# Kernel tuning notes

Measured on AMD Instinct MI355X. Metric: run time of the kernel, lower is better.

The kernel has to match this reference:

```python
import jax, jax.numpy as jnp
import numpy as np

B, S, D, H = 2, 2048, 1024, 16
DK = D // H


def setup_inputs() -> dict:
    key = jax.random.key(0)
    ks = jax.random.split(key, 12)
    lim = 1.0 / np.sqrt(D)
    def lin(kw, kb):
        W = jax.random.uniform(kw, (D, D), jnp.float32, -lim, lim)
        b = jax.random.uniform(kb, (D,), jnp.float32, -lim, lim)
        return W, b
    Wq, bq = lin(ks[0], ks[1])
    Wk, bk = lin(ks[2], ks[3])
    Wv, bv = lin(ks[4], ks[5])
    Wo, bo = lin(ks[6], ks[7])
    Q = jax.random.normal(ks[8], (B, S, D), jnp.float32)
    K = jax.random.normal(ks[9], (B, S, D), jnp.float32)
    V = jax.random.normal(ks[10], (B, S, D), jnp.float32)
    # causal mask, broadcastable to (B, H, S, S)
    mask = jnp.broadcast_to(jnp.tril(jnp.ones((S, S), jnp.bool_))[None, None], (B, 1, S, S))
    return {"Q": Q, "K": K, "V": V, "mask": mask,
            "Wq": Wq, "bq": bq, "Wk": Wk, "bk": bk,
            "Wv": Wv, "bv": bv, "Wo": Wo, "bo": bo}


def reference(Q, K, V, mask, Wq, bq, Wk, bk, Wv, bv, Wo, bo):
    def split(x):  # (B,S,D) -> (B,H,S,DK)
        return x.reshape(B, S, H, DK).transpose(0, 2, 1, 3)
    q = split(Q @ Wq.T + bq)
    k = split(K @ Wk.T + bk)
    v = split(V @ Wv.T + bv)
    scores = jnp.einsum('bhqd,bhkd->bhqk', q, k) / jnp.sqrt(jnp.float32(DK))
    scores = jnp.where(mask, scores, jnp.float32(-1e9))
    probs = jax.nn.softmax(scores, axis=-1)
    out = jnp.einsum('bhqk,bhkd->bhqd', probs, v)  # (B,H,S,DK)
    out = out.transpose(0, 2, 1, 3).reshape(B, S, D)
    return out @ Wo.T + bo
```

## Files before the change

kernel.cpp:

```cpp
#include <hip/hip_runtime.h>

#define S_LEN 2048
#define D_DIM 1024
#define H_NUM 16
#define DK_DIM 64
#define BATCH 2
#define M_TOT (BATCH * S_LEN)
#define XSZ 4194304
#define WSZ 1048576
#define SCALE_LOG2 0.18033688f

typedef __bf16 bf16x8 __attribute__((ext_vector_type(8)));
typedef float f32x4 __attribute__((ext_vector_type(4)));
typedef unsigned short u16;
typedef unsigned short u16x8 __attribute__((ext_vector_type(8)));

__device__ inline u16 f2bf(float f) {
  union { float f; unsigned u; } v; v.f = f;
  unsigned u = v.u;
  return (u16)((u + 0x7FFFu + ((u >> 16) & 1u)) >> 16);
}

typedef const __attribute__((address_space(1))) unsigned int gu32;
typedef __attribute__((address_space(3))) unsigned int lu32;
__device__ inline void glds16(const u16* g, u16* l) {
  __builtin_amdgcn_global_load_lds((gu32*)g, (lu32*)l, 16, 0, 0);
}

__global__ __launch_bounds__(256)
void convert_kernel(const float* __restrict__ Q, const float* __restrict__ K,
                    const float* __restrict__ V, const float* __restrict__ Wq,
                    const float* __restrict__ Wk, const float* __restrict__ Wv,
                    const float* __restrict__ Wo, u16* __restrict__ Xb,
                    u16* __restrict__ Wb) {
  const size_t e = ((size_t)blockIdx.x * 256 + threadIdx.x) * 8;
  const float* src;
  u16* dst;
  size_t off;
  if (e < 3ull * XSZ) {
    const int a = (int)(e >> 22);
    src = (a == 0) ? Q : (a == 1) ? K : V;
    off = e - ((size_t)a << 22);
    dst = Xb + e;
  } else {
    const size_t ew = e - 3ull * XSZ;
    const int a = (int)(ew >> 20);
    src = (a == 0) ? Wq : (a == 1) ? Wk : (a == 2) ? Wv : Wo;
    off = ew - ((size_t)a << 20);
    dst = Wb + ew;
  }
  const float4 v0 = *reinterpret_cast<const float4*>(&src[off]);
  const float4 v1 = *reinterpret_cast<const float4*>(&src[off + 4]);
  u16x8 w;
  w[0] = f2bf(v0.x); w[1] = f2bf(v0.y); w[2] = f2bf(v0.z); w[3] = f2bf(v0.w);
  w[4] = f2bf(v1.x); w[5] = f2bf(v1.y); w[6] = f2bf(v1.z); w[7] = f2bf(v1.w);
  *reinterpret_cast<u16x8*>(dst) = w;
}

__global__ __launch_bounds__(256)
void proj_kernel(const u16* __restrict__ Qb, const u16* __restrict__ Kb,
                 const u16* __restrict__ Vb, const u16* __restrict__ Wqb,
                 const u16* __restrict__ Wkb, const u16* __restrict__ Wvb,
                 const float* __restrict__ bq, const float* __restrict__ bk,
                 const float* __restrict__ bv, u16* __restrict__ qh,
                 u16* __restrict__ kh, u16* __restrict__ vt) {
  const int f = blockIdx.x + 32 * blockIdx.y + 256 * blockIdx.z;
  const int swz = (f & 7) * 96 + (f >> 3);
  const int z = swz >> 8;
  const int bx = swz & 31, by = (swz >> 5) & 7;

  const u16* A  = (z == 0) ? Qb : (z == 1) ? Kb : Vb;
  const u16* Bw = (z == 0) ? Wqb : (z == 1) ? Wkb : Wvb;
  const float* bias = (z == 0) ? bq : (z == 1) ? bk : bv;
  u16* out = (z == 0) ? qh : (z == 1) ? kh : vt;
  const float oscale = (z == 0) ? SCALE_LOG2 : 1.0f;

  __shared__ __align__(16) u16 Asm[128 * 64];
  __shared__ __align__(16) u16 Bsm[128 * 64];

  const int tid = threadIdx.x;
  const int m0 = bx * 128, n0 = by * 128;
  const int wid = tid >> 6, lane = tid & 63;
  const int col = lane & 15, quad = lane >> 4;
  const int wm = (wid >> 1) * 64, wn = (wid & 1) * 64;

  const int lr = lane >> 3;
  const int lc = (lane & 7) ^ lr;
  const u16* gA = A + (size_t)(m0 + 32 * wid + lr) * D_DIM + lc * 8;
  const u16* gB = Bw + (size_t)(n0 + 32 * wid + lr) * D_DIM + lc * 8;

  f32x4 acc[4][4];
  const f32x4 zero4 = {0.f, 0.f, 0.f, 0.f};
  for (int i = 0; i < 4; i++)
    for (int j = 0; j < 4; j++) acc[i][j] = zero4;

  for (int k0 = 0; k0 < D_DIM; k0 += 64) {
    __syncthreads();
    for (int j = 0; j < 4; j++) {
      glds16(gA + (size_t)j * 8 * D_DIM + k0, &Asm[(32 * wid + 8 * j) * 64]);
      glds16(gB + (size_t)j * 8 * D_DIM + k0, &Bsm[(32 * wid + 8 * j) * 64]);
    }
    __syncthreads();

    bf16x8 af[4][2], bfm[4][2];
    for (int i = 0; i < 4; i++) {
      const int row = wm + i * 16 + col;
      const int r7 = row & 7;
      af[i][0] = *reinterpret_cast<const bf16x8*>(&Asm[row * 64 + ((quad ^ r7) * 8)]);
      af[i][1] = *reinterpret_cast<const bf16x8*>(&Asm[row * 64 + (((quad + 4) ^ r7) * 8)]);
    }
    for (int j = 0; j < 4; j++) {
      const int row = wn + j * 16 + col;
      const int r7 = row & 7;
      bfm[j][0] = *reinterpret_cast<const bf16x8*>(&Bsm[row * 64 + ((quad ^ r7) * 8)]);
      bfm[j][1] = *reinterpret_cast<const bf16x8*>(&Bsm[row * 64 + (((quad + 4) ^ r7) * 8)]);
    }
    if (z == 2) {
      for (int h = 0; h < 2; h++)
        for (int i = 0; i < 4; i++)
          for (int j = 0; j < 4; j++)
            acc[i][j] = __builtin_amdgcn_mfma_f32_16x16x32_bf16(
                af[i][h], bfm[j][h], acc[i][j], 0, 0, 0);
    } else {
      for (int h = 0; h < 2; h++)
        for (int i = 0; i < 4; i++)
          for (int j = 0; j < 4; j++)
            acc[i][j] = __builtin_amdgcn_mfma_f32_16x16x32_bf16(
                bfm[j][h], af[i][h], acc[i][j], 0, 0, 0);
    }
  }

  if (z != 2) {
    float4 b4[4];
    for (int j = 0; j < 4; j++)
      b4[j] = *reinterpret_cast<const float4*>(&bias[n0 + wn + j * 16 + quad * 4]);
    for (int i = 0; i < 4; i++) {
      const int token = m0 + wm + i * 16 + col;
      const int b = token >> 11, s = token & (S_LEN - 1);
      for (int j = 0; j < 4; j++) {
        const int gnb = n0 + wn + j * 16 + quad * 4;
        const int h = gnb >> 6, dk = gnb & 63;
        ushort4 w;
        w.x = f2bf((acc[i][j][0] + b4[j].x) * oscale);
        w.y = f2bf((acc[i][j][1] + b4[j].y) * oscale);
        w.z = f2bf((acc[i][j][2] + b4[j].z) * oscale);
        w.w = f2bf((acc[i][j][3] + b4[j].w) * oscale);
        *reinterpret_cast<ushort4*>(
            &out[((size_t)(b * H_NUM + h) * S_LEN + s) * DK_DIM + dk]) = w;
      }
    }
  } else {
    float bb[4];
    for (int j = 0; j < 4; j++) bb[j] = bias[n0 + wn + j * 16 + col];
    for (int i = 0; i < 4; i++) {
      const int token0 = m0 + wm + i * 16 + quad * 4;
      const int b = token0 >> 11, s0 = token0 & (S_LEN - 1);
      for (int j = 0; j < 4; j++) {
        const int gn = n0 + wn + j * 16 + col;
        const int h = gn >> 6, dk = gn & 63;
        ushort4 w;
        w.x = f2bf(acc[i][j][0] + bb[j]);
        w.y = f2bf(acc[i][j][1] + bb[j]);
        w.z = f2bf(acc[i][j][2] + bb[j]);
        w.w = f2bf(acc[i][j][3] + bb[j]);
        *reinterpret_cast<ushort4*>(
            &out[((size_t)(b * H_NUM + h) * DK_DIM + dk) * S_LEN + s0]) = w;
      }
    }
  }
}

__global__ __launch_bounds__(256)
void attn_kernel(const u16* __restrict__ qh, const u16* __restrict__ kh,
                 const u16* __restrict__ vt, u16* __restrict__ ctx) {
  __shared__ __align__(16) u16 Ksm[2][64 * 64];
  __shared__ __align__(16) u16 Vsm[2][64 * 64];
  __shared__ __align__(16) u16 Psm[4][16][72];

  const int tid  = threadIdx.x;
  const int flat = blockIdx.x;
  const int qb   = 31 - (flat >> 5);
  const int bh   = flat & 31;
  const int wid  = tid >> 6;
  const int lane = tid & 63;
  const int col  = lane & 15;
  const int quad = lane >> 4;
  const int r7   = col & 7;

  const int lr = lane >> 3;
  const int lc = (lane & 7) ^ lr;
  const u16* kbase = kh + ((size_t)bh * S_LEN + 16 * wid + lr) * DK_DIM + lc * 8;
  const u16* vbase = vt + ((size_t)bh * DK_DIM + 16 * wid + lr) * S_LEN + lc * 8;

  const f32x4 zero4 = {0.f, 0.f, 0.f, 0.f};
  const int b_ = bh >> 4, h_ = bh & 15;

  const int nt = qb + 1;
  const int qrow_w = qb * 64 + wid * 16;
  const int qg = qrow_w + col;

  bf16x8 qB[2];
  {
    const u16* qp = &qh[((size_t)bh * S_LEN + qg) * DK_DIM + quad * 8];
    qB[0] = *reinterpret_cast<const bf16x8*>(qp);
    qB[1] = *reinterpret_cast<const bf16x8*>(qp + 32);
  }

  glds16(kbase, &Ksm[0][(16 * wid) * 64]);
  glds16(kbase + 8 * DK_DIM, &Ksm[0][(16 * wid + 8) * 64]);
  glds16(vbase, &Vsm[0][(16 * wid) * 64]);
  glds16(vbase + (size_t)8 * S_LEN, &Vsm[0][(16 * wid + 8) * 64]);

  float l_ = 0.f;
  f32x4 o[4];
  for (int dm = 0; dm < 4; dm++) o[dm] = zero4;

  for (int tt = 0; tt < nt; tt++) {
    const int b = tt & 1;
    __syncthreads();

    if (tt + 1 < nt) {
      const int nkv = (tt + 1) * 64;
      u16* kd = &Ksm[b ^ 1][(16 * wid) * 64];
      u16* vd = &Vsm[b ^ 1][(16 * wid) * 64];
      glds16(kbase + (size_t)nkv * DK_DIM, kd);
      glds16(kbase + (size_t)(nkv + 8) * DK_DIM, kd + 8 * 64);
      glds16(vbase + nkv, vd);
      glds16(vbase + (size_t)8 * S_LEN + nkv, vd + 8 * 64);
    }

    const int kv0 = tt * 64;
    f32x4 s[4];
    __builtin_amdgcn_s_setprio(1);
    for (int nc = 0; nc < 4; nc++) {
      const int row = nc * 16 + col;
      const bf16x8 kA0 = *reinterpret_cast<const bf16x8*>(
          &Ksm[b][row * 64 + ((quad ^ r7) * 8)]);
      const bf16x8 kA1 = *reinterpret_cast<const bf16x8*>(
          &Ksm[b][row * 64 + (((quad + 4) ^ r7) * 8)]);
      f32x4 acc = zero4;
      acc = __builtin_amdgcn_mfma_f32_16x16x32_bf16(kA0, qB[0], acc, 0, 0, 0);
      acc = __builtin_amdgcn_mfma_f32_16x16x32_bf16(kA1, qB[1], acc, 0, 0, 0);
      s[nc] = acc;
    }
    __builtin_amdgcn_s_setprio(0);

    const bool domask = (kv0 + 63 > qrow_w);
    for (int nc = 0; nc < 4; nc++) {
      const int kvb = kv0 + nc * 16 + quad * 4;
      float p[4];
      for (int r = 0; r < 4; r++) {
        float e = __builtin_amdgcn_exp2f(s[nc][r]);
        if (domask && (kvb + r > qg)) e = 0.f;
        p[r] = e;
      }
      unsigned u0 = __float_as_uint(p[0]), u1 = __float_as_uint(p[1]);
      unsigned u2 = __float_as_uint(p[2]), u3 = __float_as_uint(p[3]);
      l_ += __uint_as_float(u0 & 0xffff0000u);
      l_ += __uint_as_float(u1 & 0xffff0000u);
      l_ += __uint_as_float(u2 & 0xffff0000u);
      l_ += __uint_as_float(u3 & 0xffff0000u);
      uint2 pw;
      pw.x = __builtin_amdgcn_perm(u1, u0, 0x07060302);
      pw.y = __builtin_amdgcn_perm(u3, u2, 0x07060302);
      *reinterpret_cast<uint2*>(&Psm[wid][col][nc * 16 + quad * 4]) = pw;
    }

    asm volatile("s_waitcnt lgkmcnt(0)" ::: "memory");

    bf16x8 pB[2];
    pB[0] = *reinterpret_cast<const bf16x8*>(&Psm[wid][col][quad * 8]);
    pB[1] = *reinterpret_cast<const bf16x8*>(&Psm[wid][col][32 + quad * 8]);
    __builtin_amdgcn_s_setprio(1);
    for (int dm = 0; dm < 4; dm++) {
      const int row = dm * 16 + col;
      const bf16x8 vA0 = *reinterpret_cast<const bf16x8*>(
          &Vsm[b][row * 64 + ((quad ^ r7) * 8)]);
      const bf16x8 vA1 = *reinterpret_cast<const bf16x8*>(
          &Vsm[b][row * 64 + (((quad + 4) ^ r7) * 8)]);
      o[dm] = __builtin_amdgcn_mfma_f32_16x16x32_bf16(vA0, pB[0], o[dm], 0, 0, 0);
      o[dm] = __builtin_amdgcn_mfma_f32_16x16x32_bf16(vA1, pB[1], o[dm], 0, 0, 0);
    }
    __builtin_amdgcn_s_setprio(0);
  }

  float rs = l_;
  rs += __shfl_xor(rs, 16);
  rs += __shfl_xor(rs, 32);
  const float inv = 1.0f / rs;
  for (int dm = 0; dm < 4; dm++) {
    ushort4 w;
    w.x = f2bf(o[dm][0] * inv);
    w.y = f2bf(o[dm][1] * inv);
    w.z = f2bf(o[dm][2] * inv);
    w.w = f2bf(o[dm][3] * inv);
    *reinterpret_cast<ushort4*>(
        &ctx[((size_t)b_ * S_LEN + qg) * D_DIM + h_ * DK_DIM + dm * 16 +
             quad * 4]) = w;
  }
}

__global__ __launch_bounds__(256)
void outproj_kernel(const u16* __restrict__ ctx, const u16* __restrict__ Wob,
                    const float* __restrict__ bo, float* __restrict__ out) {
  __shared__ __align__(16) u16 Asm[2][64 * 64];
  __shared__ __align__(16) u16 Bsm[2][128 * 64];

  const int f = blockIdx.x + 64 * blockIdx.y;
  const int swz = (f & 7) * 64 + (f >> 3);
  const int m0 = (swz & 63) * 64, n0 = (swz >> 6) * 128;

  const int tid = threadIdx.x;
  const int wid = tid >> 6, lane = tid & 63;
  const int col = lane & 15, quad = lane >> 4;

  const int lr = lane >> 3;
  const int lc = (lane & 7) ^ lr;
  const u16* gA = ctx + (size_t)(m0 + 16 * wid + lr) * D_DIM + lc * 8;
  const u16* gB = Wob + (size_t)(n0 + 32 * wid + lr) * D_DIM + lc * 8;

  f32x4 acc[4][2];
  const f32x4 zero4 = {0.f, 0.f, 0.f, 0.f};
  for (int i = 0; i < 4; i++)
    for (int j = 0; j < 2; j++) acc[i][j] = zero4;

  for (int j = 0; j < 2; j++)
    glds16(gA + (size_t)j * 8 * D_DIM, &Asm[0][(16 * wid + 8 * j) * 64]);
  for (int j = 0; j < 4; j++)
    glds16(gB + (size_t)j * 8 * D_DIM, &Bsm[0][(32 * wid + 8 * j) * 64]);

  for (int ks = 0; ks < 16; ks++) {
    const int b = ks & 1;
    __syncthreads();

    if (ks + 1 < 16) {
      const int k1 = (ks + 1) * 64;
      for (int j = 0; j < 2; j++)
        glds16(gA + (size_t)j * 8 * D_DIM + k1,
               &Asm[b ^ 1][(16 * wid + 8 * j) * 64]);
      for (int j = 0; j < 4; j++)
        glds16(gB + (size_t)j * 8 * D_DIM + k1,
               &Bsm[b ^ 1][(32 * wid + 8 * j) * 64]);
    }

    bf16x8 af[4][2], bfm[2][2];
    for (int i = 0; i < 4; i++) {
      const int row = i * 16 + col;
      const int r7 = row & 7;
      af[i][0] = *reinterpret_cast<const bf16x8*>(&Asm[b][row * 64 + ((quad ^ r7) * 8)]);
      af[i][1] = *reinterpret_cast<const bf16x8*>(&Asm[b][row * 64 + (((quad + 4) ^ r7) * 8)]);
    }
    for (int j = 0; j < 2; j++) {
      const int row = 32 * wid + j * 16 + col;
      const int r7 = row & 7;
      bfm[j][0] = *reinterpret_cast<const bf16x8*>(&Bsm[b][row * 64 + ((quad ^ r7) * 8)]);
      bfm[j][1] = *reinterpret_cast<const bf16x8*>(&Bsm[b][row * 64 + (((quad + 4) ^ r7) * 8)]);
    }
    for (int h = 0; h < 2; h++)
      for (int i = 0; i < 4; i++)
        for (int j = 0; j < 2; j++)
          acc[i][j] = __builtin_amdgcn_mfma_f32_16x16x32_bf16(
              bfm[j][h], af[i][h], acc[i][j], 0, 0, 0);
  }

  float4 b4[2];
  for (int j = 0; j < 2; j++)
    b4[j] = *reinterpret_cast<const float4*>(
        &bo[n0 + 32 * wid + j * 16 + quad * 4]);
  for (int i = 0; i < 4; i++) {
    const int token = m0 + i * 16 + col;
    for (int j = 0; j < 2; j++) {
      const int gnb = n0 + 32 * wid + j * 16 + quad * 4;
      float4 v;
      v.x = acc[i][j][0] + b4[j].x;
      v.y = acc[i][j][1] + b4[j].y;
      v.z = acc[i][j][2] + b4[j].z;
      v.w = acc[i][j][3] + b4[j].w;
      *reinterpret_cast<float4*>(&out[(size_t)token * D_DIM + gnb]) = v;
    }
  }
}

extern "C" void kernel_launch(void* const* d_in, const int* in_sizes, int n_in,
                              void* d_out, int out_size, void* d_ws,
                              size_t ws_size, hipStream_t stream) {
  const float* Q  = (const float*)d_in[0];
  const float* K  = (const float*)d_in[1];
  const float* V  = (const float*)d_in[2];
  const float* Wq = (const float*)d_in[4];
  const float* bq = (const float*)d_in[5];
  const float* Wk = (const float*)d_in[6];
  const float* bk = (const float*)d_in[7];
  const float* Wv = (const float*)d_in[8];
  const float* bv = (const float*)d_in[9];
  const float* Wo = (const float*)d_in[10];
  const float* bo = (const float*)d_in[11];
  float* out = (float*)d_out;

  u16* qh  = (u16*)d_ws;
  u16* kh  = qh + XSZ;
  u16* vt  = kh + XSZ;
  u16* Qb  = vt + XSZ;
  u16* ctx = Qb;
  u16* Kb  = Qb + XSZ;
  u16* Vb  = Kb + XSZ;
  u16* Wqb = Vb + XSZ;
  u16* Wkb = Wqb + WSZ;
  u16* Wvb = Wkb + WSZ;
  u16* Wob = Wvb + WSZ;

  convert_kernel<<<(3 * XSZ + 4 * WSZ) / (256 * 8), 256, 0, stream>>>(
      Q, K, V, Wq, Wk, Wv, Wo, Qb, Wqb);

  proj_kernel<<<dim3(M_TOT / 128, D_DIM / 128, 3), 256, 0, stream>>>(
      Qb, Kb, Vb, Wqb, Wkb, Wvb, bq, bk, bv, qh, kh, vt);

  attn_kernel<<<dim3(1024), 256, 0, stream>>>(qh, kh, vt, ctx);

  outproj_kernel<<<dim3(M_TOT / 64, D_DIM / 128), 256, 0, stream>>>(ctx, Wob,
                                                                    bo, out);
}
```

Measured before the change: 260.5 us.

## Drop block swizzles, XOR-swizzle P tile, reorder causal query blocks

Removes the XCD-aware block-index swizzles in the projection and output-projection kernels and goes back to plain grid mapping. The attention kernel's P scratch tile loses its row padding and uses an XOR swizzle instead, which saves LDS while trying to keep bank conflicts low. The causal query-block order changes from strictly heaviest-first to a heavy-then-light interleaved order. The convert kernel splits its 16-byte store into two 8-byte stores. Dropping the swizzles may reduce L2 locality across XCDs, and the new query-block order may hurt tail balancing.

```diff
diff --git a/kernel.cpp b/kernel.cpp
--- a/kernel.cpp
+++ b/kernel.cpp
@@ -13,7 +13,6 @@
 typedef __bf16 bf16x8 __attribute__((ext_vector_type(8)));
 typedef float f32x4 __attribute__((ext_vector_type(4)));
 typedef unsigned short u16;
-typedef unsigned short u16x8 __attribute__((ext_vector_type(8)));
 
 __device__ inline u16 f2bf(float f) {
   union { float f; unsigned u; } v; v.f = f;
@@ -51,10 +50,11 @@
   }
   const float4 v0 = *reinterpret_cast<const float4*>(&src[off]);
   const float4 v1 = *reinterpret_cast<const float4*>(&src[off + 4]);
-  u16x8 w;
-  w[0] = f2bf(v0.x); w[1] = f2bf(v0.y); w[2] = f2bf(v0.z); w[3] = f2bf(v0.w);
-  w[4] = f2bf(v1.x); w[5] = f2bf(v1.y); w[6] = f2bf(v1.z); w[7] = f2bf(v1.w);
-  *reinterpret_cast<u16x8*>(dst) = w;
+  ushort4 w0, w1;
+  w0.x = f2bf(v0.x); w0.y = f2bf(v0.y); w0.z = f2bf(v0.z); w0.w = f2bf(v0.w);
+  w1.x = f2bf(v1.x); w1.y = f2bf(v1.y); w1.z = f2bf(v1.z); w1.w = f2bf(v1.w);
+  *reinterpret_cast<ushort4*>(dst) = w0;
+  *reinterpret_cast<ushort4*>(dst + 4) = w1;
 }
 
 __global__ __launch_bounds__(256)
@@ -64,11 +64,7 @@
                  const float* __restrict__ bq, const float* __restrict__ bk,
                  const float* __restrict__ bv, u16* __restrict__ qh,
                  u16* __restrict__ kh, u16* __restrict__ vt) {
-  const int f = blockIdx.x + 32 * blockIdx.y + 256 * blockIdx.z;
-  const int swz = (f & 7) * 96 + (f >> 3);
-  const int z = swz >> 8;
-  const int bx = swz & 31, by = (swz >> 5) & 7;
-
+  const int z = blockIdx.z;
   const u16* A  = (z == 0) ? Qb : (z == 1) ? Kb : Vb;
   const u16* Bw = (z == 0) ? Wqb : (z == 1) ? Wkb : Wvb;
   const float* bias = (z == 0) ? bq : (z == 1) ? bk : bv;
@@ -79,7 +75,7 @@
   __shared__ __align__(16) u16 Bsm[128 * 64];
 
   const int tid = threadIdx.x;
-  const int m0 = bx * 128, n0 = by * 128;
+  const int m0 = blockIdx.x * 128, n0 = blockIdx.y * 128;
   const int wid = tid >> 6, lane = tid & 63;
   const int col = lane & 15, quad = lane >> 4;
   const int wm = (wid >> 1) * 64, wn = (wid & 1) * 64;
@@ -175,17 +171,19 @@
                  const u16* __restrict__ vt, u16* __restrict__ ctx) {
   __shared__ __align__(16) u16 Ksm[2][64 * 64];
   __shared__ __align__(16) u16 Vsm[2][64 * 64];
-  __shared__ __align__(16) u16 Psm[4][16][72];
+  __shared__ __align__(16) u16 Psm[4][16][64];
 
   const int tid  = threadIdx.x;
   const int flat = blockIdx.x;
-  const int qb   = 31 - (flat >> 5);
+  const int g    = flat >> 5;
+  const int qb   = (g < 16) ? (31 - g) : (g - 16);
   const int bh   = flat & 31;
   const int wid  = tid >> 6;
   const int lane = tid & 63;
   const int col  = lane & 15;
   const int quad = lane >> 4;
   const int r7   = col & 7;
+  const int psw  = (col & 3) << 4;
 
   const int lr = lane >> 3;
   const int lc = (lane & 7) ^ lr;
@@ -263,14 +261,16 @@
       uint2 pw;
       pw.x = __builtin_amdgcn_perm(u1, u0, 0x07060302);
       pw.y = __builtin_amdgcn_perm(u3, u2, 0x07060302);
-      *reinterpret_cast<uint2*>(&Psm[wid][col][nc * 16 + quad * 4]) = pw;
+      *reinterpret_cast<uint2*>(
+          &Psm[wid][col][(nc * 16 + quad * 4) ^ psw]) = pw;
     }
 
     asm volatile("s_waitcnt lgkmcnt(0)" ::: "memory");
 
     bf16x8 pB[2];
-    pB[0] = *reinterpret_cast<const bf16x8*>(&Psm[wid][col][quad * 8]);
-    pB[1] = *reinterpret_cast<const bf16x8*>(&Psm[wid][col][32 + quad * 8]);
+    pB[0] = *reinterpret_cast<const bf16x8*>(&Psm[wid][col][(quad * 8) ^ psw]);
+    pB[1] = *reinterpret_cast<const bf16x8*>(
+        &Psm[wid][col][(32 + quad * 8) ^ psw]);
     __builtin_amdgcn_s_setprio(1);
     for (int dm = 0; dm < 4; dm++) {
       const int row = dm * 16 + col;
@@ -306,11 +306,8 @@
   __shared__ __align__(16) u16 Asm[2][64 * 64];
   __shared__ __align__(16) u16 Bsm[2][128 * 64];
 
-  const int f = blockIdx.x + 64 * blockIdx.y;
-  const int swz = (f & 7) * 64 + (f >> 3);
-  const int m0 = (swz & 63) * 64, n0 = (swz >> 6) * 128;
-
   const int tid = threadIdx.x;
+  const int m0 = blockIdx.x * 64, n0 = blockIdx.y * 128;
   const int wid = tid >> 6, lane = tid & 63;
   const int col = lane & 15, quad = lane >> 4;
 
```

New measurement: 239.9 us. -7.9%, faster.
